# Optimization experiments

Measured on AMD Instinct MI355X. Metric: run time of the kernel, lower is better.

## Reference

```python
import jax, jax.numpy as jnp
import numpy as np

# --- module constants (from init_kwargs) ---
BETA = 0.95
UTE = 1.0001
DELAY = 7
CHOSEN_W1 = 0.5
THRESHOLD = 1.0      # snntorch Leaky default threshold
ALPHA = 2.0          # snntorch ATan surrogate default alpha
T, B = 4096, 4096
SPIKE_PROB = 0.02    # sparse binary spike trains


@jax.custom_vjp
def spike_fn(x):
    # Heaviside forward; ATan surrogate gradient in backward (snntorch default)
    return (x > 0).astype(x.dtype)

def _spike_fwd(x):
    return spike_fn(x), x

def _spike_bwd(x, g):
    return (g * (ALPHA / 2.0) / (1.0 + (jnp.pi / 2.0 * ALPHA * x) ** 2),)

spike_fn.defvjp(_spike_fwd, _spike_bwd)


def setup_inputs() -> dict:
    key = jax.random.key(0)
    k1, _ = jax.random.split(key)
    spike_seq = (jax.random.uniform(k1, (T, B, 2)) < SPIKE_PROB).astype(jnp.float32)
    # calculate_weights(delay): w1 = chosen_w1; w2 = ute - beta**delay * w1
    w1 = CHOSEN_W1
    w2 = UTE - BETA ** DELAY * w1
    W = jnp.array([[w1, w2]], dtype=jnp.float32)  # fc.weight, shape [1, 2]
    return {"spike_seq": spike_seq, "W": W}


def reference(spike_seq, W):
    # spike_seq: [T, B, 2], W: [1, 2] -> spk_rec: [T, B, 1]
    # Precompute all linear currents in one GEMM (same math as per-step fc)
    cur_seq = jnp.einsum('tbi,oi->tbo', spike_seq, W)  # [T, B, 1]

    def step(mem, cur):
        # snntorch Leaky (reset_mechanism='subtract'):
        #   reset computed from PREVIOUS mem (detached heaviside)
        reset = (mem > THRESHOLD).astype(mem.dtype)
        mem_new = BETA * mem + cur - reset * THRESHOLD
        spk = spike_fn(mem_new - THRESHOLD)
        return mem_new, spk

    mem0 = jnp.zeros((spike_seq.shape[1], 1), dtype=spike_seq.dtype)
    _, spk_rec = jax.lax.scan(step, mem0, cur_seq)
    return spk_rec
```

## Files before the change

### kernel.cpp

```cpp
#include <hip/hip_runtime.h>
#include <stdint.h>


#define T_STEPS 4096
#define B_NEUR  4096
#define NCHUNK  16
#define CH_W    16
#define WARM_W  48
#define KG      (T_STEPS / 16)

typedef float f4v __attribute__((ext_vector_type(4)));

__global__ __launch_bounds__(256) void fmfm_compress(
    const f4v*  __restrict__ sp4,
    uint32_t*   __restrict__ codes)
{
    const int tid = blockIdx.x * 256 + threadIdx.x;
    const int b2  = tid & (B_NEUR / 2 - 1);
    const int kg  = tid >> 11;
    const f4v* p = sp4 + (size_t)kg * 16 * (B_NEUR / 2) + b2;
    uint32_t we = 0, wo = 0;
    #pragma unroll
    for (int i = 0; i < 16; ++i) {
        f4v s = __builtin_nontemporal_load(p + (size_t)i * (B_NEUR / 2));
        uint32_t ce = (s.x != 0.0f ? 1u : 0u) | (s.y != 0.0f ? 2u : 0u);
        uint32_t co = (s.z != 0.0f ? 1u : 0u) | (s.w != 0.0f ? 2u : 0u);
        we |= ce << (2 * i);
        wo |= co << (2 * i);
    }
    uint2 wv = make_uint2(we, wo);
    *reinterpret_cast<uint2*>(codes + (size_t)kg * B_NEUR + 2 * b2) = wv;
}

__global__ __launch_bounds__(256) void fmfm_scanA(
    const uint32_t* __restrict__ codes,
    const float*    __restrict__ W,
    float*          __restrict__ out,
    uint4*          __restrict__ spec)
{
    __shared__ float2 lut2[16];

    const float w1  = W[0];
    const float w2  = W[1];
    const float w12 = __fadd_rn(w1, w2);

    if (threadIdx.x < 16) {
        uint32_t e = threadIdx.x;
        uint32_t c0 = e & 3u, c1 = (e >> 2) & 3u;
        float2 v;
        v.x = (c0 & 1u) ? ((c0 & 2u) ? w12 : w1) : ((c0 & 2u) ? w2 : 0.0f);
        v.y = (c1 & 1u) ? ((c1 & 2u) ? w12 : w1) : ((c1 & 2u) ? w2 : 0.0f);
        lut2[e] = v;
    }
    __syncthreads();

    const int tid = blockIdx.x * 256 + threadIdx.x;
    const int b   = tid & (B_NEUR - 1);
    const int c   = tid >> 12;
    const int body_w0 = c * CH_W;
    const int w_start = (body_w0 >= WARM_W) ? body_w0 - WARM_W : 0;
    const int w_end   = body_w0 + CH_W;
    const uint32_t* cp = codes + b;

#define CLD(IDX) cp[(size_t)((IDX) < w_end ? (IDX) : (w_end - 1)) * B_NEUR]

#define DECODE2(WORD, D)                                                  \
    {                                                                     \
        _Pragma("unroll")                                                 \
        for (int _j = 0; _j < 8; ++_j)                                    \
            D[_j] = lut2[((WORD) >> (4 * _j)) & 0xFu];                    \
    }

#define STEPN(CUR)                                                        \
    {                                                                     \
        float _m = __fsub_rn(__fadd_rn(__fmul_rn(0.95f, mem), (CUR)),     \
                             rst);                                        \
        rst = (_m > 1.0f) ? 1.0f : 0.0f;                                  \
        mem = _m;                                                         \
    }

#define STEPS_(CUR, Q, K)                                                 \
    {                                                                     \
        float _m = __fsub_rn(__fadd_rn(__fmul_rn(0.95f, mem), (CUR)),     \
                             rst);                                        \
        rst = (_m > 1.0f) ? 1.0f : 0.0f;                                  \
        mem = _m;                                                         \
        __builtin_nontemporal_store(rst, (Q) + (size_t)(K) * B_NEUR);     \
    }

#define CHAIN16N(D)                                                       \
    {                                                                     \
        _Pragma("unroll")                                                 \
        for (int _j = 0; _j < 8; ++_j) { STEPN(D[_j].x) STEPN(D[_j].y) }  \
    }

#define CHAIN16S(D, WIDX)                                                 \
    {                                                                     \
        float* _q = out + (size_t)(WIDX) * 16 * B_NEUR + b;               \
        _Pragma("unroll")                                                 \
        for (int _j = 0; _j < 8; ++_j) {                                  \
            STEPS_(D[_j].x, _q, 2 * _j)                                   \
            STEPS_(D[_j].y, _q, 2 * _j + 1)                               \
        }                                                                 \
    }

    uint32_t pa = CLD(w_start);
    uint32_t pb = CLD(w_start + 1);
    uint32_t pc = CLD(w_start + 2);
    uint32_t pd = CLD(w_start + 3);

    float2 dA[8], dB[8];
    DECODE2(pa, dA)

    float mem = 0.0f, rst = 0.0f;

    for (int iw = w_start; iw < body_w0; iw += 2) {
        uint32_t t0 = CLD(iw + 4);
        DECODE2(pb, dB)
        CHAIN16N(dA)
        pa = pb; pb = pc; pc = pd; pd = t0;
        uint32_t t1 = CLD(iw + 5);
        DECODE2(pb, dA)
        CHAIN16N(dB)
        pa = pb; pb = pc; pc = pd; pd = t1;
    }

    const float sm = mem;
    const float sr = rst;

    for (int iw = body_w0; iw < w_end; iw += 2) {
        uint32_t t0 = CLD(iw + 4);
        DECODE2(pb, dB)
        CHAIN16S(dA, iw)
        pa = pb; pb = pc; pc = pd; pd = t0;
        uint32_t t1 = CLD(iw + 5);
        DECODE2(pb, dA)
        CHAIN16S(dB, iw + 1)
        pa = pb; pb = pc; pc = pd; pd = t1;
    }

    uint4 sv;
    sv.x = __float_as_uint(sm);
    sv.y = (sr != 0.0f) ? 1u : 0u;
    sv.z = __float_as_uint(mem);
    sv.w = (rst != 0.0f) ? 1u : 0u;
    spec[(size_t)c * B_NEUR + b] = sv;

#undef CLD
#undef DECODE2
#undef STEPN
#undef STEPS_
#undef CHAIN16N
#undef CHAIN16S
}

__global__ __launch_bounds__(64) void fmfm_scanB(
    const uint32_t* __restrict__ codes,
    const float*    __restrict__ W,
    float*          __restrict__ out,
    const uint4*    __restrict__ spec)
{
    const int b = blockIdx.x * 64 + threadIdx.x;
    const float w1  = W[0];
    const float w2  = W[1];
    const float w12 = __fadd_rn(w1, w2);

    float mem = 0.0f, rst = 0.0f;
    uint4 sn = spec[b];
    for (int c = 0; c < NCHUNK; ++c) {
        uint4 s = sn;
        if (c + 1 < NCHUNK) sn = spec[(size_t)(c + 1) * B_NEUR + b];
        bool ok = (s.x == __float_as_uint(mem)) &&
                  ((s.y != 0u) == (rst != 0.0f));
        if (ok) {
            mem = __uint_as_float(s.z);
            rst = s.w ? 1.0f : 0.0f;
        } else {
            for (int wi = 0; wi < CH_W; ++wi) {
                uint32_t w = codes[(size_t)(c * CH_W + wi) * B_NEUR + b];
                float* q = out + (size_t)(c * CH_W + wi) * 16 * B_NEUR + b;
                #pragma unroll
                for (int j = 0; j < 16; ++j) {
                    uint32_t cc = (w >> (2 * j)) & 3u;
                    float cur = (cc & 1u) ? ((cc & 2u) ? w12 : w1)
                                          : ((cc & 2u) ? w2 : 0.0f);
                    float m = __fsub_rn(__fadd_rn(__fmul_rn(0.95f, mem), cur),
                                        rst);
                    rst = (m > 1.0f) ? 1.0f : 0.0f;
                    mem = m;
                    q[(size_t)j * B_NEUR] = rst;
                }
            }
        }
    }
}

__global__ __launch_bounds__(64) void fmfm_scan_fused(
    const float2* __restrict__ sp, const float* __restrict__ W,
    float* __restrict__ out)
{
    const int b = blockIdx.x * 64 + threadIdx.x;
    const float w1 = W[0];
    const float w2 = W[1];
    const float2* p = sp + b;
    float* q = out + b;
    float mem = 0.0f, rst = 0.0f;
    #pragma unroll 8
    for (int t = 0; t < T_STEPS; ++t) {
        float2 s = p[(size_t)t * B_NEUR];
        float cur = __fadd_rn(__fmul_rn(s.x, w1), __fmul_rn(s.y, w2));
        float m = __fsub_rn(__fadd_rn(__fmul_rn(0.95f, mem), cur), rst);
        float spk = (m > 1.0f) ? 1.0f : 0.0f;
        q[(size_t)t * B_NEUR] = spk;
        mem = m;
        rst = spk;
    }
}

extern "C" void kernel_launch(void* const* d_in, const int* in_sizes, int n_in,
                              void* d_out, int out_size, void* d_ws, size_t ws_size,
                              hipStream_t stream) {
    const f4v*   sp4 = (const f4v*)d_in[0];
    const float* W   = (const float*)d_in[1];
    float*       out = (float*)d_out;

    const size_t codes_bytes = (size_t)KG * B_NEUR * 4;
    const size_t spec_bytes  = (size_t)NCHUNK * B_NEUR * 16;
    if (ws_size < codes_bytes + spec_bytes) {
        fmfm_scan_fused<<<dim3(B_NEUR / 64), dim3(64), 0, stream>>>(
            (const float2*)d_in[0], W, out);
        return;
    }
    uint32_t* codes = (uint32_t*)d_ws;
    uint4*    spec  = (uint4*)((char*)d_ws + codes_bytes);

    fmfm_compress<<<dim3(KG * (B_NEUR / 2) / 256), dim3(256), 0, stream>>>(sp4, codes);
    fmfm_scanA<<<dim3(NCHUNK * B_NEUR / 256), dim3(256), 0, stream>>>(codes, W, out, spec);
    fmfm_scanB<<<dim3(B_NEUR / 64), dim3(64), 0, stream>>>(codes, W, out, spec);
}
```

Baseline: 54.93 us.

## Fuse compress, scanA and scanB into one cooperative kernel with grid syncs

Merges the three kernel launches into a single cooperative kernel of 256 blocks that runs compress, chunked scan A and fix-up scan B as phases separated by grid-wide syncs. The original three kernels are kept as a fallback if the cooperative launch fails. This is meant to remove launch overhead and inter-kernel gaps. In exchange, each phase runs at reduced parallelism: compress does 8 items per thread, and scanB runs on only 16 blocks while the other blocks sit idle.

```diff
diff --git a/kernel.cpp b/kernel.cpp
--- a/kernel.cpp
+++ b/kernel.cpp
@@ -1,5 +1,8 @@
 #include <hip/hip_runtime.h>
+#include <hip/hip_cooperative_groups.h>
 #include <stdint.h>
+
+namespace cg = cooperative_groups;
 
 
 #define T_STEPS 4096
@@ -11,13 +14,11 @@
 
 typedef float f4v __attribute__((ext_vector_type(4)));
 
-__global__ __launch_bounds__(256) void fmfm_compress(
-    const f4v*  __restrict__ sp4,
-    uint32_t*   __restrict__ codes)
-{
-    const int tid = blockIdx.x * 256 + threadIdx.x;
-    const int b2  = tid & (B_NEUR / 2 - 1);
-    const int kg  = tid >> 11;
+__device__ __forceinline__ void compress_item(
+    const f4v* __restrict__ sp4, uint32_t* __restrict__ codes, int tid)
+{
+    const int b2 = tid & (B_NEUR / 2 - 1);
+    const int kg = tid >> 11;
     const f4v* p = sp4 + (size_t)kg * 16 * (B_NEUR / 2) + b2;
     uint32_t we = 0, wo = 0;
     #pragma unroll
@@ -28,49 +29,28 @@
         we |= ce << (2 * i);
         wo |= co << (2 * i);
     }
-    uint2 wv = make_uint2(we, wo);
-    *reinterpret_cast<uint2*>(codes + (size_t)kg * B_NEUR + 2 * b2) = wv;
-}
-
-__global__ __launch_bounds__(256) void fmfm_scanA(
-    const uint32_t* __restrict__ codes,
-    const float*    __restrict__ W,
-    float*          __restrict__ out,
-    uint4*          __restrict__ spec)
-{
-    __shared__ float2 lut2[16];
-
-    const float w1  = W[0];
-    const float w2  = W[1];
-    const float w12 = __fadd_rn(w1, w2);
-
-    if (threadIdx.x < 16) {
-        uint32_t e = threadIdx.x;
-        uint32_t c0 = e & 3u, c1 = (e >> 2) & 3u;
-        float2 v;
-        v.x = (c0 & 1u) ? ((c0 & 2u) ? w12 : w1) : ((c0 & 2u) ? w2 : 0.0f);
-        v.y = (c1 & 1u) ? ((c1 & 2u) ? w12 : w1) : ((c1 & 2u) ? w2 : 0.0f);
-        lut2[e] = v;
-    }
-    __syncthreads();
-
-    const int tid = blockIdx.x * 256 + threadIdx.x;
-    const int b   = tid & (B_NEUR - 1);
-    const int c   = tid >> 12;
+    *reinterpret_cast<uint2*>(codes + (size_t)kg * B_NEUR + 2 * b2) =
+        make_uint2(we, wo);
+}
+
+__device__ __forceinline__ void scanA_item(
+    const uint32_t* __restrict__ codes, float* __restrict__ out,
+    uint4* __restrict__ spec, const float2* lut2, int tid)
+{
+    const int b = tid & (B_NEUR - 1);
+    const int c = tid >> 12;
     const int body_w0 = c * CH_W;
     const int w_start = (body_w0 >= WARM_W) ? body_w0 - WARM_W : 0;
     const int w_end   = body_w0 + CH_W;
     const uint32_t* cp = codes + b;
 
 #define CLD(IDX) cp[(size_t)((IDX) < w_end ? (IDX) : (w_end - 1)) * B_NEUR]
-
 #define DECODE2(WORD, D)                                                  \
     {                                                                     \
         _Pragma("unroll")                                                 \
         for (int _j = 0; _j < 8; ++_j)                                    \
             D[_j] = lut2[((WORD) >> (4 * _j)) & 0xFu];                    \
     }
-
 #define STEPN(CUR)                                                        \
     {                                                                     \
         float _m = __fsub_rn(__fadd_rn(__fmul_rn(0.95f, mem), (CUR)),     \
@@ -78,7 +58,6 @@
         rst = (_m > 1.0f) ? 1.0f : 0.0f;                                  \
         mem = _m;                                                         \
     }
-
 #define STEPS_(CUR, Q, K)                                                 \
     {                                                                     \
         float _m = __fsub_rn(__fadd_rn(__fmul_rn(0.95f, mem), (CUR)),     \
@@ -87,13 +66,11 @@
         mem = _m;                                                         \
         __builtin_nontemporal_store(rst, (Q) + (size_t)(K) * B_NEUR);     \
     }
-
 #define CHAIN16N(D)                                                       \
     {                                                                     \
         _Pragma("unroll")                                                 \
         for (int _j = 0; _j < 8; ++_j) { STEPN(D[_j].x) STEPN(D[_j].y) }  \
     }
-
 #define CHAIN16S(D, WIDX)                                                 \
     {                                                                     \
         float* _q = out + (size_t)(WIDX) * 16 * B_NEUR + b;               \
@@ -154,17 +131,10 @@
 #undef CHAIN16S
 }
 
-__global__ __launch_bounds__(64) void fmfm_scanB(
-    const uint32_t* __restrict__ codes,
-    const float*    __restrict__ W,
-    float*          __restrict__ out,
-    const uint4*    __restrict__ spec)
-{
-    const int b = blockIdx.x * 64 + threadIdx.x;
-    const float w1  = W[0];
-    const float w2  = W[1];
-    const float w12 = __fadd_rn(w1, w2);
-
+__device__ __forceinline__ void scanB_item(
+    const uint32_t* __restrict__ codes, float w1, float w2, float w12,
+    float* __restrict__ out, const uint4* __restrict__ spec, int b)
+{
     float mem = 0.0f, rst = 0.0f;
     uint4 sn = spec[b];
     for (int c = 0; c < NCHUNK; ++c) {
@@ -195,6 +165,76 @@
     }
 }
 
+__device__ __forceinline__ void lut_init(float2* lut2, float w1, float w2,
+                                         float w12)
+{
+    if (threadIdx.x < 16) {
+        uint32_t e = threadIdx.x;
+        uint32_t c0 = e & 3u, c1 = (e >> 2) & 3u;
+        float2 v;
+        v.x = (c0 & 1u) ? ((c0 & 2u) ? w12 : w1) : ((c0 & 2u) ? w2 : 0.0f);
+        v.y = (c1 & 1u) ? ((c1 & 2u) ? w12 : w1) : ((c1 & 2u) ? w2 : 0.0f);
+        lut2[e] = v;
+    }
+}
+
+__global__ __launch_bounds__(256) void fmfm_mega(
+    const f4v*   __restrict__ sp4,
+    const float* __restrict__ W,
+    float*       __restrict__ out,
+    uint32_t*    __restrict__ codes,
+    uint4*       __restrict__ spec)
+{
+    __shared__ float2 lut2[16];
+    const float w1  = W[0];
+    const float w2  = W[1];
+    const float w12 = __fadd_rn(w1, w2);
+    lut_init(lut2, w1, w2, w12);
+    __syncthreads();
+
+    const int tid0 = blockIdx.x * 256 + threadIdx.x;
+
+    #pragma unroll
+    for (int it = 0; it < 8; ++it)
+        compress_item(sp4, codes, tid0 + it * 65536);
+
+    __threadfence();
+    cg::this_grid().sync();
+
+    scanA_item(codes, out, spec, lut2, tid0);
+
+    __threadfence();
+    cg::this_grid().sync();
+
+    if (tid0 < B_NEUR)
+        scanB_item(codes, w1, w2, w12, out, spec, tid0);
+}
+
+__global__ __launch_bounds__(256) void fmfm_compress(
+    const f4v* __restrict__ sp4, uint32_t* __restrict__ codes)
+{
+    compress_item(sp4, codes, blockIdx.x * 256 + threadIdx.x);
+}
+
+__global__ __launch_bounds__(256) void fmfm_scanA(
+    const uint32_t* __restrict__ codes, const float* __restrict__ W,
+    float* __restrict__ out, uint4* __restrict__ spec)
+{
+    __shared__ float2 lut2[16];
+    const float w1 = W[0], w2 = W[1], w12 = __fadd_rn(w1, w2);
+    lut_init(lut2, w1, w2, w12);
+    __syncthreads();
+    scanA_item(codes, out, spec, lut2, blockIdx.x * 256 + threadIdx.x);
+}
+
+__global__ __launch_bounds__(64) void fmfm_scanB(
+    const uint32_t* __restrict__ codes, const float* __restrict__ W,
+    float* __restrict__ out, const uint4* __restrict__ spec)
+{
+    const float w1 = W[0], w2 = W[1], w12 = __fadd_rn(w1, w2);
+    scanB_item(codes, w1, w2, w12, out, spec, blockIdx.x * 64 + threadIdx.x);
+}
+
 __global__ __launch_bounds__(64) void fmfm_scan_fused(
     const float2* __restrict__ sp, const float* __restrict__ W,
     float* __restrict__ out)
@@ -234,6 +274,12 @@
     uint32_t* codes = (uint32_t*)d_ws;
     uint4*    spec  = (uint4*)((char*)d_ws + codes_bytes);
 
+    void* args[] = {(void*)&sp4, (void*)&W, (void*)&out,
+                    (void*)&codes, (void*)&spec};
+    hipError_t e = hipLaunchCooperativeKernel(
+        (const void*)fmfm_mega, dim3(256), dim3(256), args, 0u, stream);
+    if (e == hipSuccess) return;
+
     fmfm_compress<<<dim3(KG * (B_NEUR / 2) / 256), dim3(256), 0, stream>>>(sp4, codes);
     fmfm_scanA<<<dim3(NCHUNK * B_NEUR / 256), dim3(256), 0, stream>>>(codes, W, out, spec);
     fmfm_scanB<<<dim3(B_NEUR / 64), dim3(64), 0, stream>>>(codes, W, out, spec);
```

Result: slower. 183.5 us (+234.1%).

## Fuse chunk fix-up pass into scan kernel via last-block ticket

Applied to the files above, without the earlier changes.

Merges the second scan pass into the first kernel. An atomic ticket lets the last block to finish run the chunk-boundary verification and any recomputation, which removes one kernel launch and its inter-kernel gap. The compress kernel resets the ticket. The fix-up now runs on a single 256-thread block rather than 64 blocks spread across the GPU, so the serial tail may be longer.

```diff
diff --git a/kernel.cpp b/kernel.cpp
--- a/kernel.cpp
+++ b/kernel.cpp
@@ -13,8 +13,10 @@
 
 __global__ __launch_bounds__(256) void fmfm_compress(
     const f4v*  __restrict__ sp4,
-    uint32_t*   __restrict__ codes)
+    uint32_t*   __restrict__ codes,
+    uint32_t*   __restrict__ ticket)
 {
+    if (blockIdx.x == 0 && threadIdx.x == 0) *ticket = 0;
     const int tid = blockIdx.x * 256 + threadIdx.x;
     const int b2  = tid & (B_NEUR / 2 - 1);
     const int kg  = tid >> 11;
@@ -28,17 +30,19 @@
         we |= ce << (2 * i);
         wo |= co << (2 * i);
     }
-    uint2 wv = make_uint2(we, wo);
-    *reinterpret_cast<uint2*>(codes + (size_t)kg * B_NEUR + 2 * b2) = wv;
-}
-
-__global__ __launch_bounds__(256) void fmfm_scanA(
+    *reinterpret_cast<uint2*>(codes + (size_t)kg * B_NEUR + 2 * b2) =
+        make_uint2(we, wo);
+}
+
+__global__ __launch_bounds__(256) void fmfm_scanAB(
     const uint32_t* __restrict__ codes,
     const float*    __restrict__ W,
     float*          __restrict__ out,
-    uint4*          __restrict__ spec)
+    uint4*          __restrict__ spec,
+    uint32_t*       __restrict__ ticket)
 {
     __shared__ float2 lut2[16];
+    __shared__ int is_last;
 
     const float w1  = W[0];
     const float w2  = W[1];
@@ -63,14 +67,12 @@
     const uint32_t* cp = codes + b;
 
 #define CLD(IDX) cp[(size_t)((IDX) < w_end ? (IDX) : (w_end - 1)) * B_NEUR]
-
 #define DECODE2(WORD, D)                                                  \
     {                                                                     \
         _Pragma("unroll")                                                 \
         for (int _j = 0; _j < 8; ++_j)                                    \
             D[_j] = lut2[((WORD) >> (4 * _j)) & 0xFu];                    \
     }
-
 #define STEPN(CUR)                                                        \
     {                                                                     \
         float _m = __fsub_rn(__fadd_rn(__fmul_rn(0.95f, mem), (CUR)),     \
@@ -78,7 +80,6 @@
         rst = (_m > 1.0f) ? 1.0f : 0.0f;                                  \
         mem = _m;                                                         \
     }
-
 #define STEPS_(CUR, Q, K)                                                 \
     {                                                                     \
         float _m = __fsub_rn(__fadd_rn(__fmul_rn(0.95f, mem), (CUR)),     \
@@ -87,13 +88,11 @@
         mem = _m;                                                         \
         __builtin_nontemporal_store(rst, (Q) + (size_t)(K) * B_NEUR);     \
     }
-
 #define CHAIN16N(D)                                                       \
     {                                                                     \
         _Pragma("unroll")                                                 \
         for (int _j = 0; _j < 8; ++_j) { STEPN(D[_j].x) STEPN(D[_j].y) }  \
     }
-
 #define CHAIN16S(D, WIDX)                                                 \
     {                                                                     \
         float* _q = out + (size_t)(WIDX) * 16 * B_NEUR + b;               \
@@ -146,53 +145,51 @@
     sv.w = (rst != 0.0f) ? 1u : 0u;
     spec[(size_t)c * B_NEUR + b] = sv;
 
+    __threadfence();
+    __syncthreads();
+    if (threadIdx.x == 0)
+        is_last = (atomicAdd(ticket, 1u) == (uint32_t)(gridDim.x - 1));
+    __syncthreads();
+    if (!is_last) return;
+    __threadfence();
+
+    for (int n = threadIdx.x; n < B_NEUR; n += 256) {
+        float vmem = 0.0f, vrst = 0.0f;
+        uint4 sn = spec[n];
+        for (int cc2 = 0; cc2 < NCHUNK; ++cc2) {
+            uint4 s = sn;
+            if (cc2 + 1 < NCHUNK) sn = spec[(size_t)(cc2 + 1) * B_NEUR + n];
+            bool ok = (s.x == __float_as_uint(vmem)) &&
+                      ((s.y != 0u) == (vrst != 0.0f));
+            if (ok) {
+                vmem = __uint_as_float(s.z);
+                vrst = s.w ? 1.0f : 0.0f;
+            } else {
+                for (int wi = 0; wi < CH_W; ++wi) {
+                    uint32_t w = codes[(size_t)(cc2 * CH_W + wi) * B_NEUR + n];
+                    float* q = out + (size_t)(cc2 * CH_W + wi) * 16 * B_NEUR + n;
+                    #pragma unroll
+                    for (int j = 0; j < 16; ++j) {
+                        uint32_t cj = (w >> (2 * j)) & 3u;
+                        float cur = (cj & 1u) ? ((cj & 2u) ? w12 : w1)
+                                              : ((cj & 2u) ? w2 : 0.0f);
+                        float m = __fsub_rn(
+                            __fadd_rn(__fmul_rn(0.95f, vmem), cur), vrst);
+                        vrst = (m > 1.0f) ? 1.0f : 0.0f;
+                        vmem = m;
+                        q[(size_t)j * B_NEUR] = vrst;
+                    }
+                }
+            }
+        }
+    }
+
 #undef CLD
 #undef DECODE2
 #undef STEPN
 #undef STEPS_
 #undef CHAIN16N
 #undef CHAIN16S
-}
-
-__global__ __launch_bounds__(64) void fmfm_scanB(
-    const uint32_t* __restrict__ codes,
-    const float*    __restrict__ W,
-    float*          __restrict__ out,
-    const uint4*    __restrict__ spec)
-{
-    const int b = blockIdx.x * 64 + threadIdx.x;
-    const float w1  = W[0];
-    const float w2  = W[1];
-    const float w12 = __fadd_rn(w1, w2);
-
-    float mem = 0.0f, rst = 0.0f;
-    uint4 sn = spec[b];
-    for (int c = 0; c < NCHUNK; ++c) {
-        uint4 s = sn;
-        if (c + 1 < NCHUNK) sn = spec[(size_t)(c + 1) * B_NEUR + b];
-        bool ok = (s.x == __float_as_uint(mem)) &&
-                  ((s.y != 0u) == (rst != 0.0f));
-        if (ok) {
-            mem = __uint_as_float(s.z);
-            rst = s.w ? 1.0f : 0.0f;
-        } else {
-            for (int wi = 0; wi < CH_W; ++wi) {
-                uint32_t w = codes[(size_t)(c * CH_W + wi) * B_NEUR + b];
-                float* q = out + (size_t)(c * CH_W + wi) * 16 * B_NEUR + b;
-                #pragma unroll
-                for (int j = 0; j < 16; ++j) {
-                    uint32_t cc = (w >> (2 * j)) & 3u;
-                    float cur = (cc & 1u) ? ((cc & 2u) ? w12 : w1)
-                                          : ((cc & 2u) ? w2 : 0.0f);
-                    float m = __fsub_rn(__fadd_rn(__fmul_rn(0.95f, mem), cur),
-                                        rst);
-                    rst = (m > 1.0f) ? 1.0f : 0.0f;
-                    mem = m;
-                    q[(size_t)j * B_NEUR] = rst;
-                }
-            }
-        }
-    }
 }
 
 __global__ __launch_bounds__(64) void fmfm_scan_fused(
@@ -226,15 +223,17 @@
 
     const size_t codes_bytes = (size_t)KG * B_NEUR * 4;
     const size_t spec_bytes  = (size_t)NCHUNK * B_NEUR * 16;
-    if (ws_size < codes_bytes + spec_bytes) {
+    if (ws_size < codes_bytes + spec_bytes + 64) {
         fmfm_scan_fused<<<dim3(B_NEUR / 64), dim3(64), 0, stream>>>(
             (const float2*)d_in[0], W, out);
         return;
     }
-    uint32_t* codes = (uint32_t*)d_ws;
-    uint4*    spec  = (uint4*)((char*)d_ws + codes_bytes);
-
-    fmfm_compress<<<dim3(KG * (B_NEUR / 2) / 256), dim3(256), 0, stream>>>(sp4, codes);
-    fmfm_scanA<<<dim3(NCHUNK * B_NEUR / 256), dim3(256), 0, stream>>>(codes, W, out, spec);
-    fmfm_scanB<<<dim3(B_NEUR / 64), dim3(64), 0, stream>>>(codes, W, out, spec);
-}
+    uint32_t* codes  = (uint32_t*)d_ws;
+    uint4*    spec   = (uint4*)((char*)d_ws + codes_bytes);
+    uint32_t* ticket = (uint32_t*)((char*)d_ws + codes_bytes + spec_bytes);
+
+    fmfm_compress<<<dim3(KG * (B_NEUR / 2) / 256), dim3(256), 0, stream>>>(
+        sp4, codes, ticket);
+    fmfm_scanAB<<<dim3(NCHUNK * B_NEUR / 256), dim3(256), 0, stream>>>(
+        codes, W, out, spec, ticket);
+}
```

New measurement: 141.7 us. +157.9%, slower.
